# Kernel tuning notes

Measured on AMD Instinct MI355X. Metric: run time of the kernel, lower is better.

The kernel has to match this reference:

```python
import jax, jax.numpy as jnp
import numpy as np

N_NODES = 100000
N_EDGES = 1600000
IN_FEATS = 128
HEADS = 4
OUT_FEATS = 16


def setup_inputs() -> dict:
    key = jax.random.key(0)
    k1, k2, k3, k4, k5 = jax.random.split(key, 5)
    x = jax.random.normal(k1, (N_NODES, IN_FEATS), dtype=jnp.float32)
    edge_index = jax.random.randint(k2, (2, N_EDGES), 0, N_NODES, dtype=jnp.int64)
    # glorot init scales
    s_w = float(np.sqrt(6.0 / (IN_FEATS + HEADS * OUT_FEATS)))
    s_a = float(np.sqrt(6.0 / (HEADS + OUT_FEATS)))
    W = jax.random.uniform(k3, (HEADS * OUT_FEATS, IN_FEATS), jnp.float32, -s_w, s_w)
    att_i = jax.random.uniform(k4, (1, HEADS, OUT_FEATS), jnp.float32, -s_a, s_a)
    att_j = jax.random.uniform(k5, (1, HEADS, OUT_FEATS), jnp.float32, -s_a, s_a)
    return {"x": x, "edge_index": edge_index, "W": W, "att_i": att_i, "att_j": att_j}


def reference(x, edge_index, W, att_i, att_j):
    N = x.shape[0]
    H, F = att_i.shape[1], att_i.shape[2]
    src = edge_index[0]  # j (source / message sender)
    dst = edge_index[1]  # i (destination / softmax segment)
    # linear projection: [N, H, F]
    h = (x @ W.T).reshape(N, H, F)
    h_j = h[src]  # [E, H, F]
    h_i = h[dst]  # [E, H, F]
    # attention logits per edge per head
    alpha = jnp.einsum('ehf,khf->eh', h_i, att_i) + jnp.einsum('ehf,khf->eh', h_j, att_j)
    alpha = jax.nn.leaky_relu(alpha, negative_slope=0.01)
    # segment softmax over incoming edges of each destination node
    amax = jax.ops.segment_max(alpha, dst, num_segments=N)  # [N, H]
    amax = jnp.where(jnp.isfinite(amax), amax, 0.0)
    ex = jnp.exp(alpha - amax[dst])
    denom = jax.ops.segment_sum(ex, dst, num_segments=N)  # [N, H]
    alpha = ex / (denom[dst] + 1e-16)
    # weighted scatter-sum aggregation
    msg = h_j * alpha[:, :, None]  # [E, H, F]
    out = jax.ops.segment_sum(msg, dst, num_segments=N)  # [N, H, F]
    return out.reshape(N, H * F)
```

## Files before the change

### kernel.cpp

```cpp
#include <hip/hip_runtime.h>

typedef __attribute__((ext_vector_type(8))) short short8;
typedef __attribute__((ext_vector_type(4))) float f32x4;

#define N_NODES 100000
#define N_EDGES 1600000
#define IN_F 128
#define OUT_ALL 64
#define HEADS 4
#define OUT_F 16
#define NTILES (N_NODES / 16)
#define BIN_BLOCKS 250
#define EPB (N_EDGES / BIN_BLOCKS)
#define TOTAL_BLOCKS 2048
#define PROJ_BLOCKS (TOTAL_BLOCKS - BIN_BLOCKS)
#define SLICE_SHIFT 8
#define SLICE_NODES 256
#define NSLICES ((N_NODES + SLICE_NODES - 1) / SLICE_NODES)
#define SEG_CAP 4608
#define QUARTER_NODES 64
#define SORT_CAP 1280

static __device__ __forceinline__ ushort f2bf(float f) {
    unsigned u = __float_as_uint(f);
    return (ushort)((u + 0x7FFF + ((u >> 16) & 1)) >> 16);
}
static __device__ __forceinline__ float bf2f(ushort b) {
    return __uint_as_float(((unsigned)b) << 16);
}
static __device__ __forceinline__ short8 pack_bf16x8(float4 f0, float4 f1) {
    union { unsigned u[4]; short8 s; } r;
    asm("v_cvt_pk_bf16_f32 %0, %1, %2" : "=v"(r.u[0]) : "v"(f0.x), "v"(f0.y));
    asm("v_cvt_pk_bf16_f32 %0, %1, %2" : "=v"(r.u[1]) : "v"(f0.z), "v"(f0.w));
    asm("v_cvt_pk_bf16_f32 %0, %1, %2" : "=v"(r.u[2]) : "v"(f1.x), "v"(f1.y));
    asm("v_cvt_pk_bf16_f32 %0, %1, %2" : "=v"(r.u[3]) : "v"(f1.z), "v"(f1.w));
    return r.s;
}

__global__ __launch_bounds__(256) void prep_kernel(
    const float* __restrict__ W, const float* __restrict__ att_i,
    const float* __restrict__ att_j, float* __restrict__ wiwj,
    int* __restrict__ scursor)
{
    int idx = blockIdx.x * 256 + threadIdx.x;
    if (idx < NSLICES) scursor[idx] = 0;
    if (idx >= IN_F * 8) return;
    int k = idx >> 3, c = idx & 7;
    int h = c & 3;
    const float* att = (c < 4) ? att_i : att_j;
    float s = 0.f;
    #pragma unroll
    for (int f = 0; f < 16; ++f)
        s += W[(size_t)(h * 16 + f) * IN_F + k] * att[h * OUT_F + f];
    wiwj[k * 8 + c] = s;
}

__global__ __launch_bounds__(256) void proj_bin_kernel(
    const float* __restrict__ x, const float* __restrict__ W,
    const float* __restrict__ wiwj, const int* __restrict__ ei,
    ushort* __restrict__ hb, float* __restrict__ ai, float* __restrict__ aj,
    int* __restrict__ scursor, int2* __restrict__ seg)
{
    __shared__ int cnt[NSLICES];
    __shared__ int gbase[NSLICES];
    __shared__ int run[NSLICES];
    __shared__ float xs[16][129];

    if (blockIdx.x < BIN_BLOCKS) {
        int base = blockIdx.x * EPB;
        const int4* __restrict__ srcp = (const int4*)(ei + base);
        const int4* __restrict__ dstp = (const int4*)(ei + N_EDGES + base);
        for (int s = threadIdx.x; s < NSLICES; s += 256) { cnt[s] = 0; run[s] = 0; }
        __syncthreads();
        for (int i = threadIdx.x; i < EPB / 4; i += 256) {
            int4 d = dstp[i];
            atomicAdd(&cnt[d.x >> SLICE_SHIFT], 1);
            atomicAdd(&cnt[d.y >> SLICE_SHIFT], 1);
            atomicAdd(&cnt[d.z >> SLICE_SHIFT], 1);
            atomicAdd(&cnt[d.w >> SLICE_SHIFT], 1);
        }
        __syncthreads();
        for (int s = threadIdx.x; s < NSLICES; s += 256) {
            int c = cnt[s];
            gbase[s] = c ? atomicAdd(&scursor[s], c) : 0;
        }
        __syncthreads();
        for (int i = threadIdx.x; i < EPB / 4; i += 256) {
            int4 sv = srcp[i];
            int4 dv = dstp[i];
            int ss, p;
            ss = dv.x >> SLICE_SHIFT; p = gbase[ss] + atomicAdd(&run[ss], 1);
            if (p < SEG_CAP) seg[(size_t)ss * SEG_CAP + p] = make_int2(sv.x, dv.x);
            ss = dv.y >> SLICE_SHIFT; p = gbase[ss] + atomicAdd(&run[ss], 1);
            if (p < SEG_CAP) seg[(size_t)ss * SEG_CAP + p] = make_int2(sv.y, dv.y);
            ss = dv.z >> SLICE_SHIFT; p = gbase[ss] + atomicAdd(&run[ss], 1);
            if (p < SEG_CAP) seg[(size_t)ss * SEG_CAP + p] = make_int2(sv.z, dv.z);
            ss = dv.w >> SLICE_SHIFT; p = gbase[ss] + atomicAdd(&run[ss], 1);
            if (p < SEG_CAP) seg[(size_t)ss * SEG_CAP + p] = make_int2(sv.w, dv.w);
        }
        return;
    }

    int bproj = blockIdx.x - BIN_BLOCKS;
    const int nproj = PROJ_BLOCKS;

    int w   = threadIdx.x >> 6;
    int l   = threadIdx.x & 63;
    int col = l & 15;
    int kg  = l >> 4;

    short8 bw[4];
    #pragma unroll
    for (int m = 0; m < 4; ++m) {
        const float* wp = W + (size_t)(w * 16 + col) * IN_F + m * 32 + kg * 8;
        float4 f0 = *(const float4*)wp;
        float4 f1 = *(const float4*)(wp + 4);
        bw[m] = pack_bf16x8(f0, f1);
    }
    short8 bwd[4];
    #pragma unroll
    for (int m = 0; m < 4; ++m) {
        float v[8];
        #pragma unroll
        for (int j = 0; j < 8; ++j)
            v[j] = (col < 8) ? wiwj[(size_t)(m * 32 + kg * 8 + j) * 8 + col] : 0.f;
        bwd[m] = pack_bf16x8(float4{v[0], v[1], v[2], v[3]},
                             float4{v[4], v[5], v[6], v[7]});
    }

    for (int t = bproj; t < NTILES; t += nproj) {
        int nodeBase = t * 16;

        __syncthreads();
        #pragma unroll
        for (int r = 0; r < 2; ++r) {
            int chunk = threadIdx.x + r * 256;
            int row = chunk >> 5, c4 = chunk & 31;
            float4 v = *(const float4*)(x + (size_t)(nodeBase + row) * IN_F + c4 * 4);
            xs[row][c4 * 4 + 0] = v.x;
            xs[row][c4 * 4 + 1] = v.y;
            xs[row][c4 * 4 + 2] = v.z;
            xs[row][c4 * 4 + 3] = v.w;
        }
        __syncthreads();

        short8 a[4];
        #pragma unroll
        for (int m = 0; m < 4; ++m) {
            const float* xr = &xs[col][m * 32 + kg * 8];
            float4 f0 = {xr[0], xr[1], xr[2], xr[3]};
            float4 f1 = {xr[4], xr[5], xr[6], xr[7]};
            a[m] = pack_bf16x8(f0, f1);
        }
        f32x4 acc = {0.f, 0.f, 0.f, 0.f};
        f32x4 accd = {0.f, 0.f, 0.f, 0.f};
        #pragma unroll
        for (int m = 0; m < 4; ++m) {
            acc  = __builtin_amdgcn_mfma_f32_16x16x32_bf16(a[m], bw[m],  acc,  0, 0, 0);
            accd = __builtin_amdgcn_mfma_f32_16x16x32_bf16(a[m], bwd[m], accd, 0, 0, 0);
        }

        #pragma unroll
        for (int r = 0; r < 4; ++r)
            hb[(size_t)(nodeBase + kg * 4 + r) * OUT_ALL + w * 16 + col] = f2bf(acc[r]);

        if (col < 4) {
            #pragma unroll
            for (int r = 0; r < 4; ++r)
                ai[(size_t)(nodeBase + kg * 4 + r) * HEADS + col] = accd[r];
        } else if (col < 8) {
            #pragma unroll
            for (int r = 0; r < 4; ++r)
                aj[(size_t)(nodeBase + kg * 4 + r) * HEADS + (col - 4)] = accd[r];
        }
    }
}

__global__ __launch_bounds__(512) void agg_kernel(
    const int2* __restrict__ seg, const int* __restrict__ scursor,
    const ushort* __restrict__ hb, const float* __restrict__ ai,
    const float* __restrict__ aj, float* __restrict__ out)
{
    __shared__ int sorted_src[SORT_CAP];
    __shared__ int cnt[QUARTER_NODES];
    __shared__ int run[QUARTER_NODES];
    __shared__ int rowptr[QUARTER_NODES + 1];

    int s       = blockIdx.x >> 2;
    int quarter = blockIdx.x & 3;
    int nbase   = (s << SLICE_SHIFT) + quarter * QUARTER_NODES;
    int total = scursor[s]; if (total > SEG_CAP) total = SEG_CAP;
    const int2* sp = seg + (size_t)s * SEG_CAP;

    for (int i = threadIdx.x; i < QUARTER_NODES; i += 512) { cnt[i] = 0; run[i] = 0; }
    __syncthreads();

    for (int i = threadIdx.x; i < total; i += 512) {
        int d = sp[i].y & (SLICE_NODES - 1);
        if ((d >> 6) == quarter) atomicAdd(&cnt[d & (QUARTER_NODES - 1)], 1);
    }
    __syncthreads();

    if (threadIdx.x < 64) {
        int l = threadIdx.x;
        int v = cnt[l];
        int inc = v;
        #pragma unroll
        for (int d = 1; d < 64; d <<= 1) {
            int t = __shfl_up(inc, d, 64);
            if (l >= d) inc += t;
        }
        rowptr[l] = inc - v;
        if (l == 63) rowptr[64] = inc;
    }
    __syncthreads();

    for (int i = threadIdx.x; i < total; i += 512) {
        int2 e = sp[i];
        int d = e.y & (SLICE_NODES - 1);
        if ((d >> 6) == quarter) {
            int lb = d & (QUARTER_NODES - 1);
            int p = rowptr[lb] + atomicAdd(&run[lb], 1);
            if (p < SORT_CAP) sorted_src[p] = e.x;
        }
    }
    __syncthreads();

    int g    = threadIdx.x >> 3;
    int sub  = threadIdx.x & 7;
    int head = sub >> 1;
    int node = nbase + g;
    if (node >= N_NODES) return;
    int beg = rowptr[g], end = rowptr[g + 1];
    if (end > SORT_CAP) end = SORT_CAP;
    float aiv = ai[(size_t)node * HEADS + head];
    float acc[8] = {0.f, 0.f, 0.f, 0.f, 0.f, 0.f, 0.f, 0.f};
    float den = 0.f;
    for (int k = beg; k < end; ++k) {
        int src = sorted_src[k];
        float av = aiv + aj[(size_t)src * HEADS + head];
        av = av > 0.f ? av : 0.01f * av;
        float ex = __expf(av);
        den += ex;
        short8 hv = *(const short8*)(hb + (size_t)src * OUT_ALL + sub * 8);
        #pragma unroll
        for (int q = 0; q < 8; ++q)
            acc[q] += ex * bf2f((ushort)hv[q]);
    }
    float inv = 1.0f / (den + 1e-16f);
    float4 o0 = {acc[0] * inv, acc[1] * inv, acc[2] * inv, acc[3] * inv};
    float4 o1 = {acc[4] * inv, acc[5] * inv, acc[6] * inv, acc[7] * inv};
    float* op = out + (size_t)node * OUT_ALL + sub * 8;
    *(float4*)op = o0;
    *(float4*)(op + 4) = o1;
}

extern "C" void kernel_launch(void* const* d_in, const int* in_sizes, int n_in,
                              void* d_out, int out_size, void* d_ws, size_t ws_size,
                              hipStream_t stream) {
    const float* x     = (const float*)d_in[0];
    const int*   ei    = (const int*)d_in[1];
    const float* W     = (const float*)d_in[2];
    const float* att_i = (const float*)d_in[3];
    const float* att_j = (const float*)d_in[4];
    float* out = (float*)d_out;

    char* ws = (char*)d_ws;
    size_t off = 0;
    auto alloc = [&](size_t bytes) {
        void* p = ws + off;
        off += (bytes + 255) & ~(size_t)255;
        return p;
    };
    ushort* hb      = (ushort*)alloc((size_t)N_NODES * OUT_ALL * 2);
    float*  ai      = (float*)alloc((size_t)N_NODES * HEADS * 4);
    float*  aj      = (float*)alloc((size_t)N_NODES * HEADS * 4);
    float*  wiwj    = (float*)alloc((size_t)IN_F * 8 * 4);
    int*    scursor = (int*)alloc((size_t)NSLICES * 4);
    int2*   seg     = (int2*)alloc((size_t)NSLICES * SEG_CAP * 8);

    prep_kernel<<<(IN_F * 8 + 255) / 256, 256, 0, stream>>>(
        W, att_i, att_j, wiwj, scursor);
    proj_bin_kernel<<<TOTAL_BLOCKS, 256, 0, stream>>>(
        x, W, wiwj, ei, hb, ai, aj, scursor, seg);
    agg_kernel<<<NSLICES * 4, 512, 0, stream>>>(seg, scursor, hb, ai, aj, out);
}
```

Measured before the change: 96.10 us.

## Split sort from aggregation, store features head-major, pack edge entries into one int

Edge bins now pack the source index and the local destination into a single 32-bit word, halving the bin traffic. The per-quarter counting sort moves into its own kernel that writes sorted sources and row pointers to global memory. Aggregation then runs one block per (chunk, head), reading head-major bf16 features and attention logits so that each head's working set is smaller and more cache-friendly. The cost is an extra kernel launch, a global round trip for the sorted lists, and each edge list being re-read once per head.

```diff
diff --git a/kernel.cpp b/kernel.cpp
--- a/kernel.cpp
+++ b/kernel.cpp
@@ -18,8 +18,8 @@
 #define SLICE_NODES 256
 #define NSLICES ((N_NODES + SLICE_NODES - 1) / SLICE_NODES)
 #define SEG_CAP 4608
-#define QUARTER_NODES 64
-#define SORT_CAP 1280
+#define NCHUNKS (NSLICES * 4)
+#define SORT_CAPQ 1280
 
 static __device__ __forceinline__ ushort f2bf(float f) {
     unsigned u = __float_as_uint(f);
@@ -58,8 +58,8 @@
 __global__ __launch_bounds__(256) void proj_bin_kernel(
     const float* __restrict__ x, const float* __restrict__ W,
     const float* __restrict__ wiwj, const int* __restrict__ ei,
-    ushort* __restrict__ hb, float* __restrict__ ai, float* __restrict__ aj,
-    int* __restrict__ scursor, int2* __restrict__ seg)
+    ushort* __restrict__ hbg, float* __restrict__ aih, float* __restrict__ ajh,
+    int* __restrict__ scursor, int* __restrict__ seg)
 {
     __shared__ int cnt[NSLICES];
     __shared__ int gbase[NSLICES];
@@ -90,13 +90,13 @@
             int4 dv = dstp[i];
             int ss, p;
             ss = dv.x >> SLICE_SHIFT; p = gbase[ss] + atomicAdd(&run[ss], 1);
-            if (p < SEG_CAP) seg[(size_t)ss * SEG_CAP + p] = make_int2(sv.x, dv.x);
+            if (p < SEG_CAP) seg[(size_t)ss * SEG_CAP + p] = (sv.x << 8) | (dv.x & 255);
             ss = dv.y >> SLICE_SHIFT; p = gbase[ss] + atomicAdd(&run[ss], 1);
-            if (p < SEG_CAP) seg[(size_t)ss * SEG_CAP + p] = make_int2(sv.y, dv.y);
+            if (p < SEG_CAP) seg[(size_t)ss * SEG_CAP + p] = (sv.y << 8) | (dv.y & 255);
             ss = dv.z >> SLICE_SHIFT; p = gbase[ss] + atomicAdd(&run[ss], 1);
-            if (p < SEG_CAP) seg[(size_t)ss * SEG_CAP + p] = make_int2(sv.z, dv.z);
+            if (p < SEG_CAP) seg[(size_t)ss * SEG_CAP + p] = (sv.z << 8) | (dv.z & 255);
             ss = dv.w >> SLICE_SHIFT; p = gbase[ss] + atomicAdd(&run[ss], 1);
-            if (p < SEG_CAP) seg[(size_t)ss * SEG_CAP + p] = make_int2(sv.w, dv.w);
+            if (p < SEG_CAP) seg[(size_t)ss * SEG_CAP + p] = (sv.w << 8) | (dv.w & 255);
         }
         return;
     }
@@ -162,42 +162,39 @@
 
         #pragma unroll
         for (int r = 0; r < 4; ++r)
-            hb[(size_t)(nodeBase + kg * 4 + r) * OUT_ALL + w * 16 + col] = f2bf(acc[r]);
-
-        if (col < 4) {
+            hbg[((size_t)w * N_NODES + nodeBase + kg * 4 + r) * OUT_F + col] = f2bf(acc[r]);
+
+        if (col == w) {
             #pragma unroll
             for (int r = 0; r < 4; ++r)
-                ai[(size_t)(nodeBase + kg * 4 + r) * HEADS + col] = accd[r];
-        } else if (col < 8) {
+                aih[(size_t)w * N_NODES + nodeBase + kg * 4 + r] = accd[r];
+        } else if (col == w + 4) {
             #pragma unroll
             for (int r = 0; r < 4; ++r)
-                aj[(size_t)(nodeBase + kg * 4 + r) * HEADS + (col - 4)] = accd[r];
-        }
-    }
-}
-
-__global__ __launch_bounds__(512) void agg_kernel(
-    const int2* __restrict__ seg, const int* __restrict__ scursor,
-    const ushort* __restrict__ hb, const float* __restrict__ ai,
-    const float* __restrict__ aj, float* __restrict__ out)
+                ajh[(size_t)w * N_NODES + nodeBase + kg * 4 + r] = accd[r];
+        }
+    }
+}
+
+__global__ __launch_bounds__(256) void sort_kernel(
+    const int* __restrict__ seg, const int* __restrict__ scursor,
+    int* __restrict__ srt, int* __restrict__ rowptrq)
 {
-    __shared__ int sorted_src[SORT_CAP];
-    __shared__ int cnt[QUARTER_NODES];
-    __shared__ int run[QUARTER_NODES];
-    __shared__ int rowptr[QUARTER_NODES + 1];
-
-    int s       = blockIdx.x >> 2;
-    int quarter = blockIdx.x & 3;
-    int nbase   = (s << SLICE_SHIFT) + quarter * QUARTER_NODES;
+    __shared__ int cnt[64];
+    __shared__ int run[64];
+    __shared__ int rowptr[65];
+
+    int s = blockIdx.x >> 2;
+    int q = blockIdx.x & 3;
     int total = scursor[s]; if (total > SEG_CAP) total = SEG_CAP;
-    const int2* sp = seg + (size_t)s * SEG_CAP;
-
-    for (int i = threadIdx.x; i < QUARTER_NODES; i += 512) { cnt[i] = 0; run[i] = 0; }
+    const int* sp = seg + (size_t)s * SEG_CAP;
+
+    if (threadIdx.x < 64) { cnt[threadIdx.x] = 0; run[threadIdx.x] = 0; }
     __syncthreads();
 
-    for (int i = threadIdx.x; i < total; i += 512) {
-        int d = sp[i].y & (SLICE_NODES - 1);
-        if ((d >> 6) == quarter) atomicAdd(&cnt[d & (QUARTER_NODES - 1)], 1);
+    for (int i = threadIdx.x; i < total; i += 256) {
+        int d8 = sp[i] & 255;
+        if ((d8 >> 6) == q) atomicAdd(&cnt[d8 & 63], 1);
     }
     __syncthreads();
 
@@ -215,44 +212,57 @@
     }
     __syncthreads();
 
-    for (int i = threadIdx.x; i < total; i += 512) {
-        int2 e = sp[i];
-        int d = e.y & (SLICE_NODES - 1);
-        if ((d >> 6) == quarter) {
-            int lb = d & (QUARTER_NODES - 1);
+    for (int i = threadIdx.x; i < total; i += 256) {
+        int e = sp[i];
+        int d8 = e & 255;
+        if ((d8 >> 6) == q) {
+            int lb = d8 & 63;
             int p = rowptr[lb] + atomicAdd(&run[lb], 1);
-            if (p < SORT_CAP) sorted_src[p] = e.x;
+            if (p < SORT_CAPQ) srt[(size_t)blockIdx.x * SORT_CAPQ + p] = (unsigned)e >> 8;
         }
     }
     __syncthreads();
 
-    int g    = threadIdx.x >> 3;
-    int sub  = threadIdx.x & 7;
-    int head = sub >> 1;
-    int node = nbase + g;
+    if (threadIdx.x < 65) {
+        int v = rowptr[threadIdx.x];
+        rowptrq[(size_t)blockIdx.x * 65 + threadIdx.x] = v > SORT_CAPQ ? SORT_CAPQ : v;
+    }
+}
+
+__global__ __launch_bounds__(256) void agg_kernel(
+    const int* __restrict__ srt, const int* __restrict__ rowptrq,
+    const ushort* __restrict__ hbg, const float* __restrict__ aih,
+    const float* __restrict__ ajh, float* __restrict__ out)
+{
+    int chunk = blockIdx.x >> 2;
+    int head  = blockIdx.x & 3;
+    int g     = threadIdx.x >> 2;
+    int lane  = threadIdx.x & 3;
+    int node  = chunk * 64 + g;
     if (node >= N_NODES) return;
-    int beg = rowptr[g], end = rowptr[g + 1];
-    if (end > SORT_CAP) end = SORT_CAP;
-    float aiv = ai[(size_t)node * HEADS + head];
-    float acc[8] = {0.f, 0.f, 0.f, 0.f, 0.f, 0.f, 0.f, 0.f};
-    float den = 0.f;
+
+    const int* rp = rowptrq + (size_t)chunk * 65;
+    int beg = rp[g], end = rp[g + 1];
+    const int* sb = srt + (size_t)chunk * SORT_CAPQ;
+    const ushort* hb_h = hbg + (size_t)head * N_NODES * OUT_F;
+    const float*  aj_h = ajh + (size_t)head * N_NODES;
+
+    float aiv = aih[(size_t)head * N_NODES + node];
+    float4 acc = {0.f, 0.f, 0.f, 0.f};
+    float  den = 0.f;
     for (int k = beg; k < end; ++k) {
-        int src = sorted_src[k];
-        float av = aiv + aj[(size_t)src * HEADS + head];
+        int src = sb[k];
+        float av = aiv + aj_h[src];
         av = av > 0.f ? av : 0.01f * av;
         float ex = __expf(av);
         den += ex;
-        short8 hv = *(const short8*)(hb + (size_t)src * OUT_ALL + sub * 8);
-        #pragma unroll
-        for (int q = 0; q < 8; ++q)
-            acc[q] += ex * bf2f((ushort)hv[q]);
+        ushort4 hv = *(const ushort4*)(hb_h + (size_t)src * OUT_F + lane * 4);
+        acc.x += ex * bf2f(hv.x); acc.y += ex * bf2f(hv.y);
+        acc.z += ex * bf2f(hv.z); acc.w += ex * bf2f(hv.w);
     }
     float inv = 1.0f / (den + 1e-16f);
-    float4 o0 = {acc[0] * inv, acc[1] * inv, acc[2] * inv, acc[3] * inv};
-    float4 o1 = {acc[4] * inv, acc[5] * inv, acc[6] * inv, acc[7] * inv};
-    float* op = out + (size_t)node * OUT_ALL + sub * 8;
-    *(float4*)op = o0;
-    *(float4*)(op + 4) = o1;
+    acc.x *= inv; acc.y *= inv; acc.z *= inv; acc.w *= inv;
+    *(float4*)(out + (size_t)node * OUT_ALL + head * OUT_F + lane * 4) = acc;
 }
 
 extern "C" void kernel_launch(void* const* d_in, const int* in_sizes, int n_in,
@@ -272,16 +282,19 @@
         off += (bytes + 255) & ~(size_t)255;
         return p;
     };
-    ushort* hb      = (ushort*)alloc((size_t)N_NODES * OUT_ALL * 2);
-    float*  ai      = (float*)alloc((size_t)N_NODES * HEADS * 4);
-    float*  aj      = (float*)alloc((size_t)N_NODES * HEADS * 4);
+    ushort* hbg     = (ushort*)alloc((size_t)HEADS * N_NODES * OUT_F * 2);
+    float*  aih     = (float*)alloc((size_t)HEADS * N_NODES * 4);
+    float*  ajh     = (float*)alloc((size_t)HEADS * N_NODES * 4);
     float*  wiwj    = (float*)alloc((size_t)IN_F * 8 * 4);
     int*    scursor = (int*)alloc((size_t)NSLICES * 4);
-    int2*   seg     = (int2*)alloc((size_t)NSLICES * SEG_CAP * 8);
+    int*    seg     = (int*)alloc((size_t)NSLICES * SEG_CAP * 4);
+    int*    srt     = (int*)alloc((size_t)NCHUNKS * SORT_CAPQ * 4);
+    int*    rowptrq = (int*)alloc((size_t)NCHUNKS * 65 * 4);
 
     prep_kernel<<<(IN_F * 8 + 255) / 256, 256, 0, stream>>>(
         W, att_i, att_j, wiwj, scursor);
     proj_bin_kernel<<<TOTAL_BLOCKS, 256, 0, stream>>>(
-        x, W, wiwj, ei, hb, ai, aj, scursor, seg);
-    agg_kernel<<<NSLICES * 4, 512, 0, stream>>>(seg, scursor, hb, ai, aj, out);
-}
+        x, W, wiwj, ei, hbg, aih, ajh, scursor, seg);
+    sort_kernel<<<NCHUNKS, 256, 0, stream>>>(seg, scursor, srt, rowptrq);
+    agg_kernel<<<NCHUNKS * 4, 256, 0, stream>>>(srt, rowptrq, hbg, aih, ajh, out);
+}
```

Result: slower. 153.8 us (+60.0%).
